# Kernel tuning notes

Measured on AMD Instinct MI355X. Metric: run time of the kernel, lower is better.

Reference implementation:

```python
import jax, jax.numpy as jnp
import numpy as np

N_NODES = 20000
N_EDGES = 320000
IN_CH = 256
HID = 128
HEADS = 4
OUT_CH = 200
NUM_GRAPHS = 64
NEG_SLOPE = 0.2


def setup_inputs() -> dict:
    key = jax.random.key(0)
    ks = jax.random.split(key, 16)
    x = jax.random.normal(ks[0], (N_NODES, IN_CH), dtype=jnp.float32)
    edge_index = jax.random.randint(ks[1], (2, N_EDGES), 0, N_NODES, dtype=jnp.int64)
    batch = jnp.sort(jax.random.randint(ks[2], (N_NODES,), 0, NUM_GRAPHS, dtype=jnp.int64))

    def lin(k, fan_in, fan_out):
        return jax.random.normal(k, (fan_in, fan_out), dtype=jnp.float32) / np.sqrt(fan_in)

    def att(k, h, c):
        return jax.random.normal(k, (h, c), dtype=jnp.float32) / np.sqrt(c)

    return {
        "x": x, "edge_index": edge_index, "batch": batch,
        "W1": lin(ks[3], IN_CH, HEADS * HID),
        "a_src1": att(ks[4], HEADS, HID), "a_dst1": att(ks[5], HEADS, HID),
        "b1": jnp.zeros((HEADS * HID,), jnp.float32),
        "W2": lin(ks[6], HEADS * HID, HEADS * HID),
        "a_src2": att(ks[7], HEADS, HID), "a_dst2": att(ks[8], HEADS, HID),
        "b2": jnp.zeros((HEADS * HID,), jnp.float32),
        "W3": lin(ks[9], HEADS * HID, HID),
        "a_src3": att(ks[10], 1, HID), "a_dst3": att(ks[11], 1, HID),
        "b3": jnp.zeros((HID,), jnp.float32),
        "fc_w": lin(ks[12], HID, OUT_CH),
        "fc_b": jnp.zeros((OUT_CH,), jnp.float32),
    }


def gat_conv(x, src, dst, W, a_src, a_dst, bias):
    """PyG GATConv (concat=True, negative_slope=0.2, self-loops appended by caller)."""
    N = x.shape[0]
    heads, out_ch = a_src.shape
    h = (x @ W).reshape(N, heads, out_ch)                 # [N,H,C]
    alpha_s = jnp.einsum('nhc,hc->nh', h, a_src)          # [N,H]
    alpha_d = jnp.einsum('nhc,hc->nh', h, a_dst)
    e = jax.nn.leaky_relu(alpha_s[src] + alpha_d[dst], NEG_SLOPE)  # [E,H]
    # segment softmax over edges sharing the same target node
    m = jax.ops.segment_max(e, dst, num_segments=N)
    e = jnp.exp(e - m[dst])
    denom = jax.ops.segment_sum(e, dst, num_segments=N)
    alpha = e / (denom[dst] + 1e-16)                      # [E,H]
    msg = h[src] * alpha[:, :, None]                      # [E,H,C]
    out = jax.ops.segment_sum(msg, dst, num_segments=N)   # [N,H,C]
    return out.reshape(N, heads * out_ch) + bias


def reference(x, edge_index, batch, W1, a_src1, a_dst1, b1,
              W2, a_src2, a_dst2, b2, W3, a_src3, a_dst3, b3, fc_w, fc_b):
    N = x.shape[0]
    loop = jnp.arange(N, dtype=edge_index.dtype)
    src = jnp.concatenate([edge_index[0], loop])
    dst = jnp.concatenate([edge_index[1], loop])

    h = jax.nn.elu(gat_conv(x, src, dst, W1, a_src1, a_dst1, b1))
    h = jax.nn.elu(gat_conv(h, src, dst, W2, a_src2, a_dst2, b2))
    h = jax.nn.elu(gat_conv(h, src, dst, W3, a_src3, a_dst3, b3))

    # global_mean_pool over graph ids
    sums = jax.ops.segment_sum(h, batch, num_segments=NUM_GRAPHS)
    cnts = jax.ops.segment_sum(jnp.ones((N,), h.dtype), batch, num_segments=NUM_GRAPHS)
    pooled = sums / jnp.maximum(cnts, 1.0)[:, None]       # [G,HID]
    # F.dropout with training=False is identity
    logits = pooled @ fc_w + fc_b                          # [G,OUT_CH]
    return logits
```

## Files before the change

kernel.cpp:

```cpp
#include <hip/hip_runtime.h>
#include <hip/hip_bf16.h>
#include <stdint.h>

#define N_NODES   20000
#define N_EDGES   320000
#define E_TOT     (N_EDGES + N_NODES)
#define IN_CH     256
#define HID       128
#define HEADS     4
#define OUT_CH    200
#define NUM_GRAPHS 64
#define M_PAD     20096

typedef __bf16 bf16_t;
typedef __bf16 bf16x8 __attribute__((ext_vector_type(8)));
typedef __bf16 bf16x2 __attribute__((ext_vector_type(2)));
typedef float  f32x4  __attribute__((ext_vector_type(4)));

__device__ __forceinline__ bool detect_bf16(const unsigned short* __restrict__ xu16) {
  int lane = threadIdx.x & 63;
  unsigned short v = xu16[2 * lane];
  int e = (v >> 7) & 0xff;
  unsigned long long b = __ballot(e >= 90 && e <= 160);
  return __popcll(b) >= 40;
}
__device__ __forceinline__ bool detect_i64(const unsigned* __restrict__ eidx) {
  int lane = threadIdx.x & 63;
  unsigned long long b = __ballot(eidx[2 * lane + 1] == 0u);
  return __popcll(b) >= 32;
}

__global__ void cvt_x(const void* __restrict__ src, bf16_t* __restrict__ dst, int n,
                      const unsigned short* __restrict__ xu16) {
  bool isbf = detect_bf16(xu16);
  int i = blockIdx.x * 256 + threadIdx.x;
  if (i >= n) return;
  dst[i] = isbf ? ((const bf16_t*)src)[i] : (bf16_t)((const float*)src)[i];
}

struct SmallCvt {
  const void* src[11];
  bf16_t* dst[11];
  int n[11];
};

__global__ void cvt_wts(const void* __restrict__ W1, const void* __restrict__ W2,
                        const void* __restrict__ W3, bf16_t* __restrict__ W1T,
                        bf16_t* __restrict__ W2T, bf16_t* __restrict__ W3T,
                        SmallCvt tab, const unsigned short* __restrict__ xu16) {
  bool isbf = detect_bf16(xu16);
  int i = blockIdx.x * 256 + threadIdx.x;
  if (i < 131072) {
    int k = i >> 9, nn = i & 511;
    bf16_t v = isbf ? ((const bf16_t*)W1)[i] : (bf16_t)((const float*)W1)[i];
    W1T[(size_t)nn * 256 + k] = v;
  } else if (i < 131072 + 262144) {
    int i2 = i - 131072;
    int k = i2 >> 9, nn = i2 & 511;
    bf16_t v = isbf ? ((const bf16_t*)W2)[i2] : (bf16_t)((const float*)W2)[i2];
    W2T[(size_t)nn * 512 + k] = v;
  } else if (i < 131072 + 262144 + 65536) {
    int i3 = i - 131072 - 262144;
    int k = i3 >> 7, nn = i3 & 127;
    bf16_t v = isbf ? ((const bf16_t*)W3)[i3] : (bf16_t)((const float*)W3)[i3];
    W3T[(size_t)nn * 512 + k] = v;
  } else {
    int j = i - 458752;
    for (int s = 0; s < 11; ++s) {
      if (j < tab.n[s]) {
        tab.dst[s][j] = isbf ? ((const bf16_t*)tab.src[s])[j]
                             : (bf16_t)((const float*)tab.src[s])[j];
        break;
      }
      j -= tab.n[s];
    }
  }
}

__global__ void cvt_ints_hist(const int* __restrict__ eidx, const int* __restrict__ batch,
                              int* __restrict__ esrc, int* __restrict__ edst,
                              int* __restrict__ b32, int* __restrict__ deg,
                              const unsigned* __restrict__ eidx_u) {
  bool i64 = detect_i64(eidx_u);
  int i = blockIdx.x * 256 + threadIdx.x;
  if (i < N_EDGES) {
    int s = i64 ? eidx[2 * i] : eidx[i];
    int d = i64 ? eidx[2 * (N_EDGES + i)] : eidx[N_EDGES + i];
    esrc[i] = s;
    edst[i] = d;
    atomicAdd(&deg[d], 1);
  }
  if (i < N_NODES) {
    b32[i] = i64 ? batch[2 * i] : batch[i];
    atomicAdd(&deg[i], 1);
  }
}

__launch_bounds__(1024)
__global__ void scan_deg(const int* __restrict__ deg, int* __restrict__ off,
                         int* __restrict__ cursor) {
  __shared__ int wsum[16];
  __shared__ int carry_s;
  int t = threadIdx.x;
  int lane = t & 63, wid = t >> 6;
  if (t == 0) { carry_s = 0; off[0] = 0; }
  __syncthreads();
  for (int base = 0; base < N_NODES; base += 1024) {
    int i = base + t;
    int v = (i < N_NODES) ? deg[i] : 0;
    int x = v;
    for (int d = 1; d < 64; d <<= 1) {
      int y = __shfl_up(x, d);
      if (lane >= d) x += y;
    }
    if (lane == 63) wsum[wid] = x;
    __syncthreads();
    if (t < 16) {
      int y = wsum[t];
      for (int d = 1; d < 16; d <<= 1) {
        int z = __shfl_up(y, d);
        if (t >= d) y += z;
      }
      wsum[t] = y;
    }
    __syncthreads();
    int carry = carry_s;
    int prefix = (wid > 0 ? wsum[wid - 1] : 0) + carry;
    int incl = prefix + x;
    if (i < N_NODES) { off[i + 1] = incl; cursor[i] = 0; }
    __syncthreads();
    if (t == 0) carry_s = carry + wsum[15];
    __syncthreads();
  }
}

__global__ void scatter_kernel(const int* __restrict__ esrc, const int* __restrict__ edst,
                               const int* __restrict__ off, int* __restrict__ cursor,
                               int* __restrict__ csr_src) {
  int e = blockIdx.x * 256 + threadIdx.x;
  if (e >= E_TOT) return;
  int s, d;
  if (e < N_EDGES) { s = esrc[e]; d = edst[e]; } else { s = d = e - N_EDGES; }
  int pos = off[d] + atomicAdd(&cursor[d], 1);
  csr_src[pos] = s;
}

__launch_bounds__(256)
__global__ void gemm_bf16(const bf16_t* __restrict__ A, const bf16_t* __restrict__ BT,
                          bf16_t* __restrict__ C, int M, int N, int K) {
  __shared__ bf16_t As[128 * 32];
  __shared__ bf16_t Bs[128 * 32];
  const int tid  = threadIdx.x;
  const int lane = tid & 63;
  const int w    = tid >> 6;
  const int wm   = w & 1, wn = w >> 1;
  const int bm   = blockIdx.x * 128;
  const int bn   = blockIdx.y * 128;
  const int quad = lane >> 4;
  const int l16  = lane & 15;

  f32x4 zero = {0.f, 0.f, 0.f, 0.f};
  f32x4 acc[4][4];
  for (int i = 0; i < 4; ++i)
    for (int j = 0; j < 4; ++j) acc[i][j] = zero;

  const int c0 = tid, c1 = tid + 256;
  const int r0 = c0 >> 2, s0 = c0 & 3;
  const int r1 = c1 >> 2, s1 = c1 & 3;
  int ga0 = bm + r0; if (ga0 > M - 1) ga0 = M - 1;
  int ga1 = bm + r1; if (ga1 > M - 1) ga1 = M - 1;

  for (int k0 = 0; k0 < K; k0 += 32) {
    bf16x8 va0 = *(const bf16x8*)(A + (size_t)ga0 * K + k0 + s0 * 8);
    bf16x8 vb0 = *(const bf16x8*)(BT + (size_t)(bn + r0) * K + k0 + s0 * 8);
    bf16x8 va1 = *(const bf16x8*)(A + (size_t)ga1 * K + k0 + s1 * 8);
    bf16x8 vb1 = *(const bf16x8*)(BT + (size_t)(bn + r1) * K + k0 + s1 * 8);
    __syncthreads();
    *(bf16x8*)(As + c0 * 8) = va0;
    *(bf16x8*)(Bs + c0 * 8) = vb0;
    *(bf16x8*)(As + c1 * 8) = va1;
    *(bf16x8*)(Bs + c1 * 8) = vb1;
    __syncthreads();

    bf16x8 af[4], bfr[4];
    for (int mt = 0; mt < 4; ++mt) {
      int m_local = wm * 64 + mt * 16 + l16;
      af[mt] = *(const bf16x8*)(As + m_local * 32 + quad * 8);
    }
    for (int nt = 0; nt < 4; ++nt) {
      int n_local = wn * 64 + nt * 16 + l16;
      bfr[nt] = *(const bf16x8*)(Bs + n_local * 32 + quad * 8);
    }
    for (int mt = 0; mt < 4; ++mt)
      for (int nt = 0; nt < 4; ++nt)
        acc[mt][nt] = __builtin_amdgcn_mfma_f32_16x16x32_bf16(af[mt], bfr[nt], acc[mt][nt], 0, 0, 0);
  }

  for (int mt = 0; mt < 4; ++mt) {
    for (int r = 0; r < 4; ++r) {
      int m = bm + wm * 64 + mt * 16 + quad * 4 + r;
      if (m >= M) continue;
      for (int nt = 0; nt < 4; ++nt) {
        int n = bn + wn * 64 + nt * 16 + l16;
        C[(size_t)m * N + n] = (bf16_t)acc[mt][nt][r];
      }
    }
  }
}

template<int CPL>
__launch_bounds__(256)
__global__ void alpha_k(const bf16_t* __restrict__ h, const bf16_t* __restrict__ a_src,
                        const bf16_t* __restrict__ a_dst, float* __restrict__ as,
                        float* __restrict__ ad, int H) {
  typedef __bf16 vec_t __attribute__((ext_vector_type(CPL)));
  const int C = CPL * 64;
  int lane = threadIdx.x & 63;
  int n = blockIdx.x * 4 + (threadIdx.x >> 6);
  if (n >= N_NODES) return;
  int c0 = lane * CPL;
  vec_t hv  = *(const vec_t*)(h + (size_t)n * C + c0);
  vec_t sv  = *(const vec_t*)(a_src + c0);
  vec_t dv  = *(const vec_t*)(a_dst + c0);
  float s = 0.f, d = 0.f;
  for (int j = 0; j < CPL; ++j) {
    float hvf = (float)hv[j];
    s += hvf * (float)sv[j];
    d += hvf * (float)dv[j];
  }
  const int lph = 128 / CPL;
  for (int o = 1; o < lph; o <<= 1) {
    s += __shfl_xor(s, o);
    d += __shfl_xor(d, o);
  }
  if ((lane & (lph - 1)) == 0) {
    int hd = c0 >> 7;
    as[n * H + hd] = s;
    ad[n * H + hd] = d;
  }
}

template<int CPL>
__launch_bounds__(256)
__global__ void agg_fused(const bf16_t* __restrict__ h, const int* __restrict__ off,
                          const int* __restrict__ csr_src, const float* __restrict__ as,
                          const float* __restrict__ ad, const bf16_t* __restrict__ bias,
                          bf16_t* __restrict__ outp, int H) {
  typedef __bf16 vec_t __attribute__((ext_vector_type(CPL)));
  const int C = CPL * 64;
  int lane = threadIdx.x & 63;
  int n = blockIdx.x * 4 + (threadIdx.x >> 6);
  if (n >= N_NODES) return;
  int start = __builtin_amdgcn_readfirstlane(off[n]);
  int end   = __builtin_amdgcn_readfirstlane(off[n + 1]);
  int c0 = lane * CPL;
  int hd = c0 >> 7;
  float adv = ad[n * H + hd];
  float acc[CPL];
  for (int j = 0; j < CPL; ++j) acc[j] = 0.f;
  float den = 0.f;

  int pos = start;
  for (; pos + 1 < end; pos += 2) {
    int s0 = __builtin_amdgcn_readfirstlane(csr_src[pos]);
    int s1 = __builtin_amdgcn_readfirstlane(csr_src[pos + 1]);
    vec_t hv0 = *(const vec_t*)(h + (size_t)s0 * C + c0);
    vec_t hv1 = *(const vec_t*)(h + (size_t)s1 * C + c0);
    float e0 = as[s0 * H + hd] + adv; e0 = e0 > 0.f ? e0 : 0.2f * e0;
    float e1 = as[s1 * H + hd] + adv; e1 = e1 > 0.f ? e1 : 0.2f * e1;
    float w0 = __expf(e0), w1 = __expf(e1);
    den += w0 + w1;
    for (int j = 0; j < CPL; ++j)
      acc[j] += w0 * (float)hv0[j] + w1 * (float)hv1[j];
  }
  if (pos < end) {
    int s0 = __builtin_amdgcn_readfirstlane(csr_src[pos]);
    vec_t hv0 = *(const vec_t*)(h + (size_t)s0 * C + c0);
    float e0 = as[s0 * H + hd] + adv; e0 = e0 > 0.f ? e0 : 0.2f * e0;
    float w0 = __expf(e0);
    den += w0;
    for (int j = 0; j < CPL; ++j) acc[j] += w0 * (float)hv0[j];
  }

  float inv = 1.f / (den + 1e-16f);
  vec_t ov;
  for (int j = 0; j < CPL; ++j) {
    float o = acc[j] * inv + (float)bias[c0 + j];
    o = o > 0.f ? o : expm1f(o);
    ov[j] = (bf16_t)o;
  }
  *(vec_t*)(outp + (size_t)n * C + c0) = ov;
}

__launch_bounds__(256)
__global__ void pool_fc(const bf16_t* __restrict__ h3, const int* __restrict__ batch,
                        const bf16_t* __restrict__ fcw, const bf16_t* __restrict__ fcb,
                        void* __restrict__ outp, const unsigned short* __restrict__ xu16) {
  bool isbf = detect_bf16(xu16);
  int g = blockIdx.x;
  int lo = 0, hi = N_NODES;
  while (lo < hi) { int mid = (lo + hi) >> 1; if (batch[mid] < g) lo = mid + 1; else hi = mid; }
  int start = lo;
  hi = N_NODES;
  while (lo < hi) { int mid = (lo + hi) >> 1; if (batch[mid] < g + 1) lo = mid + 1; else hi = mid; }
  int end = lo;
  __shared__ float pooled[HID];
  int t = threadIdx.x;
  if (t < HID) {
    float s = 0.f;
    for (int n = start; n < end; ++n) s += (float)h3[(size_t)n * HID + t];
    int cnt = end - start;
    pooled[t] = s / (float)(cnt > 0 ? cnt : 1);
  }
  __syncthreads();
  if (t < OUT_CH) {
    float a = (float)fcb[t];
    for (int c = 0; c < HID; ++c) a += pooled[c] * (float)fcw[c * OUT_CH + t];
    if (isbf) ((bf16_t*)outp)[g * OUT_CH + t] = (bf16_t)a;
    else      ((float*)outp)[g * OUT_CH + t] = a;
  }
}

extern "C" void kernel_launch(void* const* d_in, const int* in_sizes, int n_in,
                              void* d_out, int out_size, void* d_ws, size_t ws_size,
                              hipStream_t stream) {
  const void* x    = d_in[0];
  const void* eidx = d_in[1];
  const void* batch= d_in[2];
  const void* W1   = d_in[3];
  const void* a_s1 = d_in[4];
  const void* a_d1 = d_in[5];
  const void* b1   = d_in[6];
  const void* W2   = d_in[7];
  const void* a_s2 = d_in[8];
  const void* a_d2 = d_in[9];
  const void* b2   = d_in[10];
  const void* W3   = d_in[11];
  const void* a_s3 = d_in[12];
  const void* a_d3 = d_in[13];
  const void* b3   = d_in[14];
  const void* fcw  = d_in[15];
  const void* fcb  = d_in[16];
  const unsigned short* xu16 = (const unsigned short*)x;

  char* p = (char*)d_ws;
  auto carve = [&](size_t nbytes) { char* r = p; p += (nbytes + 255) & ~(size_t)255; return r; };
  bf16_t*   W1T    = (bf16_t*)carve((size_t)512 * 256 * 2);
  bf16_t*   W2T    = (bf16_t*)carve((size_t)512 * 512 * 2);
  bf16_t*   W3T    = (bf16_t*)carve((size_t)128 * 512 * 2);
  bf16_t*   hA     = (bf16_t*)carve((size_t)M_PAD * 512 * 2);
  bf16_t*   hB     = (bf16_t*)carve((size_t)M_PAD * 512 * 2);
  bf16_t*   xb     = hB;
  bf16_t*   sm     = (bf16_t*)carve((size_t)32768 * 2);
  bf16_t *as1b = sm, *ad1b = sm + 512, *b1b = sm + 1024,
         *as2b = sm + 1536, *ad2b = sm + 2048, *b2b = sm + 2560,
         *as3b = sm + 3072, *ad3b = sm + 3200, *b3b = sm + 3328,
         *fcwb = sm + 3456, *fcbb = sm + 29056;
  float*    asb    = (float*)carve((size_t)N_NODES * 4 * 4);
  float*    adb    = (float*)carve((size_t)N_NODES * 4 * 4);
  int*      deg    = (int*)carve((size_t)N_NODES * 4);
  int*      off    = (int*)carve((size_t)(N_NODES + 1) * 4);
  int*      cursor = (int*)carve((size_t)N_NODES * 4);
  int*      csr_src= (int*)carve((size_t)E_TOT * 4);
  int*      esrc32 = (int*)carve((size_t)N_EDGES * 4);
  int*      edst32 = (int*)carve((size_t)N_EDGES * 4);
  int*      bat32  = (int*)carve((size_t)N_NODES * 4);

  dim3 b256(256);
  const int NG4 = (N_NODES + 3) / 4;

  hipMemsetAsync(deg, 0, (size_t)N_NODES * 4, stream);
  cvt_x<<<dim3((N_NODES * IN_CH + 255) / 256), b256, 0, stream>>>(x, xb, N_NODES * IN_CH, xu16);
  SmallCvt tab;
  const void* srcs[11] = {a_s1, a_d1, b1, a_s2, a_d2, b2, a_s3, a_d3, b3, fcw, fcb};
  bf16_t* dsts[11] = {as1b, ad1b, b1b, as2b, ad2b, b2b, as3b, ad3b, b3b, fcwb, fcbb};
  int ns[11] = {512, 512, 512, 512, 512, 512, 128, 128, 128, 25600, 200};
  for (int i = 0; i < 11; ++i) { tab.src[i] = srcs[i]; tab.dst[i] = dsts[i]; tab.n[i] = ns[i]; }
  cvt_wts<<<dim3((458752 + 29256 + 255) / 256), b256, 0, stream>>>(W1, W2, W3, W1T, W2T, W3T, tab, xu16);
  cvt_ints_hist<<<dim3((N_EDGES + 255) / 256), b256, 0, stream>>>(
      (const int*)eidx, (const int*)batch, esrc32, edst32, bat32, deg, (const unsigned*)eidx);

  scan_deg<<<dim3(1), dim3(1024), 0, stream>>>(deg, off, cursor);
  scatter_kernel<<<dim3((E_TOT + 255) / 256), b256, 0, stream>>>(esrc32, edst32, off, cursor, csr_src);

  gemm_bf16<<<dim3(157, 4), b256, 0, stream>>>(xb, W1T, hA, N_NODES, 512, 256);
  alpha_k<8><<<dim3(NG4), b256, 0, stream>>>(hA, as1b, ad1b, asb, adb, 4);
  agg_fused<8><<<dim3(NG4), b256, 0, stream>>>(hA, off, csr_src, asb, adb, b1b, hB, 4);

  gemm_bf16<<<dim3(157, 4), b256, 0, stream>>>(hB, W2T, hA, N_NODES, 512, 512);
  alpha_k<8><<<dim3(NG4), b256, 0, stream>>>(hA, as2b, ad2b, asb, adb, 4);
  agg_fused<8><<<dim3(NG4), b256, 0, stream>>>(hA, off, csr_src, asb, adb, b2b, hB, 4);

  gemm_bf16<<<dim3(157, 1), b256, 0, stream>>>(hB, W3T, hA, N_NODES, 128, 512);
  alpha_k<2><<<dim3(NG4), b256, 0, stream>>>(hA, as3b, ad3b, asb, adb, 1);
  agg_fused<2><<<dim3(NG4), b256, 0, stream>>>(hA, off, csr_src, asb, adb, b3b, hB, 1);

  pool_fc<<<dim3(NUM_GRAPHS), b256, 0, stream>>>(hB, bat32, fcwb, fcbb, d_out, xu16);
}
```

Before: 441.2 us.

## Parallelize global mean pool with per-block partial sums and atomics

Replaces the per-graph pooling kernel, which had 64 blocks walking each graph's nodes serially, with a node-parallel partial-sum kernel. That kernel accumulates runs of the same graph id per wave and flushes them to a global buffer with float atomics. Graph node counts are now computed during the int conversion pass, and a separate small kernel does the division and the final FC. This removes the long serial reduction, at the cost of an extra launch and nondeterministic float summation order.

```diff
diff --git a/kernel.cpp b/kernel.cpp
--- a/kernel.cpp
+++ b/kernel.cpp
@@ -31,9 +31,12 @@
 }
 
 __global__ void cvt_x(const void* __restrict__ src, bf16_t* __restrict__ dst, int n,
-                      const unsigned short* __restrict__ xu16) {
+                      const unsigned short* __restrict__ xu16,
+                      float* __restrict__ psums, int* __restrict__ pcnt) {
   bool isbf = detect_bf16(xu16);
   int i = blockIdx.x * 256 + threadIdx.x;
+  if (i < NUM_GRAPHS * HID) psums[i] = 0.f;
+  if (i < NUM_GRAPHS) pcnt[i] = 0;
   if (i >= n) return;
   dst[i] = isbf ? ((const bf16_t*)src)[i] : (bf16_t)((const float*)src)[i];
 }
@@ -80,6 +83,7 @@
 __global__ void cvt_ints_hist(const int* __restrict__ eidx, const int* __restrict__ batch,
                               int* __restrict__ esrc, int* __restrict__ edst,
                               int* __restrict__ b32, int* __restrict__ deg,
+                              int* __restrict__ pcnt,
                               const unsigned* __restrict__ eidx_u) {
   bool i64 = detect_i64(eidx_u);
   int i = blockIdx.x * 256 + threadIdx.x;
@@ -91,7 +95,9 @@
     atomicAdd(&deg[d], 1);
   }
   if (i < N_NODES) {
-    b32[i] = i64 ? batch[2 * i] : batch[i];
+    int g = i64 ? batch[2 * i] : batch[i];
+    b32[i] = g;
+    atomicAdd(&pcnt[g], 1);
     atomicAdd(&deg[i], 1);
   }
 }
@@ -293,24 +299,45 @@
 }
 
 __launch_bounds__(256)
-__global__ void pool_fc(const bf16_t* __restrict__ h3, const int* __restrict__ batch,
-                        const bf16_t* __restrict__ fcw, const bf16_t* __restrict__ fcb,
-                        void* __restrict__ outp, const unsigned short* __restrict__ xu16) {
+__global__ void pool_partial(const bf16_t* __restrict__ h3, const int* __restrict__ batch,
+                             float* __restrict__ psums) {
+  int wave = threadIdx.x >> 6;
+  int lane = threadIdx.x & 63;
+  int c0 = lane * 2;
+  int nbase = blockIdx.x * 128;
+  int nend = nbase + 128; if (nend > N_NODES) nend = N_NODES;
+  float a0 = 0.f, a1 = 0.f;
+  int cur = -1;
+  for (int n = nbase + wave; n < nend; n += 4) {
+    int g = __builtin_amdgcn_readfirstlane(batch[n]);
+    if (g != cur) {
+      if (cur >= 0) {
+        atomicAdd(&psums[cur * HID + c0], a0);
+        atomicAdd(&psums[cur * HID + c0 + 1], a1);
+      }
+      cur = g; a0 = 0.f; a1 = 0.f;
+    }
+    bf16x2 v = *(const bf16x2*)(h3 + (size_t)n * HID + c0);
+    a0 += (float)v[0];
+    a1 += (float)v[1];
+  }
+  if (cur >= 0) {
+    atomicAdd(&psums[cur * HID + c0], a0);
+    atomicAdd(&psums[cur * HID + c0 + 1], a1);
+  }
+}
+
+__launch_bounds__(256)
+__global__ void fc_final(const float* __restrict__ psums, const int* __restrict__ pcnt,
+                         const bf16_t* __restrict__ fcw, const bf16_t* __restrict__ fcb,
+                         void* __restrict__ outp, const unsigned short* __restrict__ xu16) {
   bool isbf = detect_bf16(xu16);
   int g = blockIdx.x;
-  int lo = 0, hi = N_NODES;
-  while (lo < hi) { int mid = (lo + hi) >> 1; if (batch[mid] < g) lo = mid + 1; else hi = mid; }
-  int start = lo;
-  hi = N_NODES;
-  while (lo < hi) { int mid = (lo + hi) >> 1; if (batch[mid] < g + 1) lo = mid + 1; else hi = mid; }
-  int end = lo;
   __shared__ float pooled[HID];
   int t = threadIdx.x;
   if (t < HID) {
-    float s = 0.f;
-    for (int n = start; n < end; ++n) s += (float)h3[(size_t)n * HID + t];
-    int cnt = end - start;
-    pooled[t] = s / (float)(cnt > 0 ? cnt : 1);
+    int c = pcnt[g];
+    pooled[t] = psums[g * HID + t] / (float)(c > 0 ? c : 1);
   }
   __syncthreads();
   if (t < OUT_CH) {
@@ -365,12 +392,15 @@
   int*      esrc32 = (int*)carve((size_t)N_EDGES * 4);
   int*      edst32 = (int*)carve((size_t)N_EDGES * 4);
   int*      bat32  = (int*)carve((size_t)N_NODES * 4);
+  float*    psums  = (float*)carve((size_t)NUM_GRAPHS * HID * 4);
+  int*      pcnt   = (int*)carve((size_t)NUM_GRAPHS * 4);
 
   dim3 b256(256);
   const int NG4 = (N_NODES + 3) / 4;
 
   hipMemsetAsync(deg, 0, (size_t)N_NODES * 4, stream);
-  cvt_x<<<dim3((N_NODES * IN_CH + 255) / 256), b256, 0, stream>>>(x, xb, N_NODES * IN_CH, xu16);
+  cvt_x<<<dim3((N_NODES * IN_CH + 255) / 256), b256, 0, stream>>>(x, xb, N_NODES * IN_CH,
+                                                                  xu16, psums, pcnt);
   SmallCvt tab;
   const void* srcs[11] = {a_s1, a_d1, b1, a_s2, a_d2, b2, a_s3, a_d3, b3, fcw, fcb};
   bf16_t* dsts[11] = {as1b, ad1b, b1b, as2b, ad2b, b2b, as3b, ad3b, b3b, fcwb, fcbb};
@@ -378,7 +408,7 @@
   for (int i = 0; i < 11; ++i) { tab.src[i] = srcs[i]; tab.dst[i] = dsts[i]; tab.n[i] = ns[i]; }
   cvt_wts<<<dim3((458752 + 29256 + 255) / 256), b256, 0, stream>>>(W1, W2, W3, W1T, W2T, W3T, tab, xu16);
   cvt_ints_hist<<<dim3((N_EDGES + 255) / 256), b256, 0, stream>>>(
-      (const int*)eidx, (const int*)batch, esrc32, edst32, bat32, deg, (const unsigned*)eidx);
+      (const int*)eidx, (const int*)batch, esrc32, edst32, bat32, deg, pcnt, (const unsigned*)eidx);
 
   scan_deg<<<dim3(1), dim3(1024), 0, stream>>>(deg, off, cursor);
   scatter_kernel<<<dim3((E_TOT + 255) / 256), b256, 0, stream>>>(esrc32, edst32, off, cursor, csr_src);
@@ -395,5 +425,6 @@
   alpha_k<2><<<dim3(NG4), b256, 0, stream>>>(hA, as3b, ad3b, asb, adb, 1);
   agg_fused<2><<<dim3(NG4), b256, 0, stream>>>(hA, off, csr_src, asb, adb, b3b, hB, 1);
 
-  pool_fc<<<dim3(NUM_GRAPHS), b256, 0, stream>>>(hB, bat32, fcwb, fcbb, d_out, xu16);
-}
+  pool_partial<<<dim3((N_NODES + 127) / 128), b256, 0, stream>>>(hB, bat32, psums);
+  fc_final<<<dim3(NUM_GRAPHS), b256, 0, stream>>>(psums, pcnt, fcwb, fcbb, d_out, xu16);
+}
```

Result: slower. 470.9 us (+6.7%).
